# Optimization experiments

Measured on AMD Instinct MI355X. Metric: run time of the kernel, lower is better.

The kernel has to match this reference:

```python
import jax, jax.numpy as jnp
import numpy as np

B, S, D, H = 2, 2048, 1024, 16
DK = D // H

def setup_inputs() -> dict:
    key = jax.random.key(0)
    ks = jax.random.split(key, 11)
    scale = 1.0 / np.sqrt(D)
    inp = {
        'query': jax.random.normal(ks[0], (B, S, D), jnp.float32),
        'key':   jax.random.normal(ks[1], (B, S, D), jnp.float32),
        'value': jax.random.normal(ks[2], (B, S, D), jnp.float32),
        'wq': jax.random.normal(ks[3], (D, D), jnp.float32) * scale,
        'bq': jax.random.normal(ks[4], (D,), jnp.float32) * 0.01,
        'wk': jax.random.normal(ks[5], (D, D), jnp.float32) * scale,
        'bk': jax.random.normal(ks[6], (D,), jnp.float32) * 0.01,
        'wv': jax.random.normal(ks[7], (D, D), jnp.float32) * scale,
        'bv': jax.random.normal(ks[8], (D,), jnp.float32) * 0.01,
        'wo': jax.random.normal(ks[9], (D, D), jnp.float32) * scale,
        'bo': jax.random.normal(ks[10], (D,), jnp.float32) * 0.01,
    }
    return inp

def reference(query, key, value, wq, bq, wk, bk, wv, bv, wo, bo):
    nb = query.shape[0]
    # projections: torch nn.Linear computes x @ W^T + b; here weights stored as (in,out)
    def proj(x, w, b):
        return (x @ w + b).reshape(nb, -1, H, DK).transpose(0, 2, 1, 3)  # [B,H,S,dk]
    q = proj(query, wq, bq)
    k = proj(key, wk, bk)
    v = proj(value, wv, bv)
    scores = jnp.einsum('bhqd,bhkd->bhqk', q, k) / jnp.sqrt(jnp.float32(DK))
    p = jax.nn.softmax(scores, axis=-1)  # dropout p=0 (eval)
    x = jnp.einsum('bhqk,bhkd->bhqd', p, v)
    x = x.transpose(0, 2, 1, 3).reshape(nb, -1, H * DK)
    return x @ wo + bo
```

## Files before the change

kernel.cpp:

```cpp
#include <hip/hip_runtime.h>


typedef __attribute__((ext_vector_type(8))) __bf16 bf16x8;
typedef __attribute__((ext_vector_type(4))) __bf16 bf16x4;
typedef __attribute__((ext_vector_type(8))) float f32x8;
typedef __attribute__((ext_vector_type(4))) float f32x4;
typedef __attribute__((ext_vector_type(16))) float f32x16;
typedef unsigned uv2 __attribute__((ext_vector_type(2)));

#define MFMA16 __builtin_amdgcn_mfma_f32_16x16x32_bf16
#define MFMA32 __builtin_amdgcn_mfma_f32_32x32x16_bf16

union Bf8 { bf16x8 v; __bf16 e[8]; };

__device__ inline f32x4 zero4() { f32x4 z; z[0]=z[1]=z[2]=z[3]=0.f; return z; }
__device__ inline f32x16 zero16() {
    f32x16 z;
#pragma unroll
    for (int i = 0; i < 16; i++) z[i] = 0.f;
    return z;
}

__device__ inline float fast_exp2(float x) {
#if __has_builtin(__builtin_amdgcn_exp2f)
    return __builtin_amdgcn_exp2f(x);
#else
    return __expf(x * 0.6931471805599453f);
#endif
}

#if __has_builtin(__builtin_amdgcn_permlane32_swap)
#define HAVE_PLSWAP 1
#endif

__device__ inline void plswap32(unsigned &a, unsigned &b) {
#ifdef HAVE_PLSWAP
    uv2 r = __builtin_amdgcn_permlane32_swap(a, b, false, false);
    a = r[0]; b = r[1];
#else
    unsigned sa = __shfl_xor((int)a, 32), sb = __shfl_xor((int)b, 32);
    bool hi = (threadIdx.x & 32) != 0;
    unsigned na = hi ? sb : a;
    unsigned nb = hi ? b : sa;
    a = na; b = nb;
#endif
}

__device__ inline float red32_max(float x) {
#ifdef HAVE_PLSWAP
    unsigned a = __float_as_uint(x), b = __float_as_uint(x);
    uv2 r = __builtin_amdgcn_permlane32_swap(a, b, false, false);
    return fmaxf(__uint_as_float(r[0]), __uint_as_float(r[1]));
#else
    return fmaxf(x, __shfl_xor(x, 32));
#endif
}
__device__ inline float red32_sum(float x) {
#ifdef HAVE_PLSWAP
    unsigned a = __float_as_uint(x), b = __float_as_uint(x);
    uv2 r = __builtin_amdgcn_permlane32_swap(a, b, false, false);
    return __uint_as_float(r[0]) + __uint_as_float(r[1]);
#else
    return x + __shfl_xor(x, 32);
#endif
}

__device__ inline unsigned pk2(float a, float b) {
    union { unsigned u; __bf16 e[2]; } r;
    r.e[0] = (__bf16)a; r.e[1] = (__bf16)b;
    return r.u;
}

__device__ inline void load_lds16(const void* g, void* l) {
    __builtin_amdgcn_global_load_lds(
        (const __attribute__((address_space(1))) unsigned int*)g,
        (__attribute__((address_space(3))) unsigned int*)l, 16, 0, 0);
}

__global__ __launch_bounds__(256) void prep_all(
        const float* __restrict__ w0, const float* __restrict__ w1,
        const float* __restrict__ w2, const float* __restrict__ w3,
        const float* __restrict__ x0, const float* __restrict__ x1,
        const float* __restrict__ x2,
        __bf16* __restrict__ wt, __bf16* __restrict__ d0,
        __bf16* __restrict__ d1, __bf16* __restrict__ d2) {
    const int z = blockIdx.z, t = threadIdx.x;
    if (z < 4) {
        const float* src = z == 0 ? w0 : z == 1 ? w1 : z == 2 ? w2 : w3;
        __bf16* dst = wt + (size_t)z * 1048576;
        __shared__ float tile[32][33];
        const int tc = t & 31, tr = t >> 5;
        const int r0 = blockIdx.y * 32, c0 = blockIdx.x * 32;
#pragma unroll
        for (int i = 0; i < 4; i++) {
            int r = tr + i * 8;
            tile[r][tc] = src[(size_t)(r0 + r) * 1024 + c0 + tc];
        }
        __syncthreads();
#pragma unroll
        for (int i = 0; i < 4; i++) {
            int r = tr + i * 8;
            dst[(size_t)(c0 + r) * 1024 + r0 + tc] = (__bf16)tile[tc][r];
        }
    } else {
        const float* src = z == 4 ? x0 : z == 5 ? x1 : x2;
        __bf16* dst = z == 4 ? d0 : z == 5 ? d1 : d2;
        int bid = blockIdx.y * 32 + blockIdx.x;
        size_t g = ((size_t)bid * 256 + t) * 16;
#pragma unroll
        for (int h = 0; h < 2; h++) {
            f32x8 a = *(const f32x8*)&src[g + h * 8];
            Bf8 tmp;
#pragma unroll
            for (int j = 0; j < 8; j++) tmp.e[j] = (__bf16)a[j];
            *(bf16x8*)&dst[g + h * 8] = tmp.v;
        }
    }
}

template <int MODE, typename OutT>
__device__ inline void gemm_fast_core(__bf16* __restrict__ smem,
                                      const __bf16* __restrict__ A,
                                      const __bf16* __restrict__ Bt,
                                      const float* __restrict__ bias,
                                      OutT* __restrict__ out, float scale) {
    __bf16* As = smem;
    __bf16* Bs = smem + 8192;
    const int t = threadIdx.x;
    const int wave = t >> 6, lane = t & 63, lm = lane & 15, quad = lane >> 4;
    const int m0 = blockIdx.y * 128, n0 = blockIdx.x * 128;
    const int wm = (wave >> 1) * 64, wn = (wave & 1) * 64;

    f32x4 acc[4][4];
#pragma unroll
    for (int i = 0; i < 4; i++)
#pragma unroll
        for (int j = 0; j < 4; j++) acc[i][j] = zero4();

    for (int k0 = 0; k0 < 1024; k0 += 64) {
#pragma unroll
        for (int i = 0; i < 4; i++) {
            int s = i * 256 + t;
            int row = s >> 3, cb = (s & 7) ^ (row & 7);
            size_t goff = (size_t)row * 1024 + k0 + cb * 8;
            load_lds16(&A[(size_t)m0 * 1024 + goff],
                       &As[(size_t)(i * 256 + wave * 64) * 8]);
            load_lds16(&Bt[(size_t)n0 * 1024 + goff],
                       &Bs[(size_t)(i * 256 + wave * 64) * 8]);
        }
        __syncthreads();
#pragma unroll
        for (int ks = 0; ks < 2; ks++) {
            bf16x8 af[4], bfr[4];
#pragma unroll
            for (int mt = 0; mt < 4; mt++)
                af[mt] = *(const bf16x8*)&As[(wm + mt * 16 + lm) * 64 +
                                             (((ks * 4 + quad) ^ (lm & 7)) * 8)];
#pragma unroll
            for (int nt = 0; nt < 4; nt++)
                bfr[nt] = *(const bf16x8*)&Bs[(wn + nt * 16 + lm) * 64 +
                                              (((ks * 4 + quad) ^ (lm & 7)) * 8)];
#pragma unroll
            for (int mt = 0; mt < 4; mt++)
#pragma unroll
                for (int nt = 0; nt < 4; nt++)
                    acc[mt][nt] = MFMA16(af[mt], bfr[nt], acc[mt][nt], 0, 0, 0);
        }
        __syncthreads();
    }

    float bv4[4];
#pragma unroll
    for (int nt = 0; nt < 4; nt++) bv4[nt] = bias[n0 + wn + nt * 16 + lm];

    if (MODE == 2) {
#pragma unroll
        for (int mt = 0; mt < 4; mt++)
#pragma unroll
            for (int r = 0; r < 4; r++) {
                int rr = wm + mt * 16 + quad * 4 + r;
#pragma unroll
                for (int nt = 0; nt < 4; nt++) {
                    int c = wn + nt * 16 + lm;
                    smem[c * 128 + (rr ^ (8 * (c & 15)))] =
                        (__bf16)((acc[mt][nt][r] + bv4[nt]) * scale);
                }
            }
        __syncthreads();
        const int b = m0 >> 11;
#pragma unroll
        for (int it = 0; it < 8; it++) {
            int g = it * 256 + t;
            int c = g >> 4, gr = g & 15;
            bf16x8 v = *(const bf16x8*)&smem[c * 128 + ((gr * 8) ^ (8 * (c & 15)))];
            int col = n0 + c, hh = col >> 6, dk = col & 63;
            int sglob = (m0 & 2047) + gr * 8;
            size_t idx = (size_t)(b * 16 + hh) * 131072 + (size_t)dk * 2048 + sglob;
            *(bf16x8*)&out[idx] = v;
        }
    } else {
#pragma unroll
        for (int mt = 0; mt < 4; mt++) {
#pragma unroll
            for (int r = 0; r < 4; r++) {
                int row = m0 + wm + mt * 16 + quad * 4 + r;
#pragma unroll
                for (int nt = 0; nt < 4; nt++) {
                    int col = n0 + wn + nt * 16 + lm;
                    float val = (acc[mt][nt][r] + bv4[nt]) * scale;
                    size_t idx;
                    if (MODE == 0) {
                        idx = (size_t)row * 1024 + col;
                    } else {
                        int b = row >> 11, s = row & 2047, hh = col >> 6, dk = col & 63;
                        idx = (size_t)(b * 16 + hh) * 131072 + (size_t)s * 64 + dk;
                    }
                    out[idx] = (OutT)val;
                }
            }
        }
    }
}

__global__ __launch_bounds__(256) void proj_fast3(
        const __bf16* __restrict__ xq, const __bf16* __restrict__ xk,
        const __bf16* __restrict__ xv, const __bf16* __restrict__ WT,
        const float* __restrict__ bq, const float* __restrict__ bk,
        const float* __restrict__ bv,
        __bf16* __restrict__ Q, __bf16* __restrict__ K, __bf16* __restrict__ Vt) {
    __shared__ __bf16 smem[16384];
    int z = blockIdx.z;
    if (z == 0)
        gemm_fast_core<1, __bf16>(smem, xq, WT, bq, Q, 0.18033688f);
    else if (z == 1)
        gemm_fast_core<1, __bf16>(smem, xk, WT + 1048576, bk, K, 1.f);
    else
        gemm_fast_core<2, __bf16>(smem, xv, WT + 2097152, bv, Vt, 1.f);
}

__global__ __launch_bounds__(256) void out_proj_fast64(
        const __bf16* __restrict__ A, const __bf16* __restrict__ Bt,
        const float* __restrict__ bias, float* __restrict__ out) {
    __shared__ __bf16 As[8192];
    __shared__ __bf16 Bs[4096];
    const int t = threadIdx.x;
    const int wave = t >> 6, lane = t & 63, lm = lane & 15, quad = lane >> 4;
    const int m0 = blockIdx.y * 128, n0 = blockIdx.x * 64;
    const int wm = (wave >> 1) * 64, wn = (wave & 1) * 32;

    f32x4 acc[4][2];
#pragma unroll
    for (int i = 0; i < 4; i++) { acc[i][0] = zero4(); acc[i][1] = zero4(); }

    for (int k0 = 0; k0 < 1024; k0 += 64) {
#pragma unroll
        for (int i = 0; i < 4; i++) {
            int s = i * 256 + t;
            int row = s >> 3, cb = (s & 7) ^ (row & 7);
            load_lds16(&A[(size_t)(m0 + row) * 1024 + k0 + cb * 8],
                       &As[(size_t)(i * 256 + wave * 64) * 8]);
            if (i < 2)
                load_lds16(&Bt[(size_t)(n0 + row) * 1024 + k0 + cb * 8],
                           &Bs[(size_t)(i * 256 + wave * 64) * 8]);
        }
        __syncthreads();
#pragma unroll
        for (int ks = 0; ks < 2; ks++) {
            bf16x8 af[4], bfr[2];
#pragma unroll
            for (int mt = 0; mt < 4; mt++)
                af[mt] = *(const bf16x8*)&As[(wm + mt * 16 + lm) * 64 +
                                             (((ks * 4 + quad) ^ (lm & 7)) * 8)];
#pragma unroll
            for (int nt = 0; nt < 2; nt++)
                bfr[nt] = *(const bf16x8*)&Bs[(wn + nt * 16 + lm) * 64 +
                                              (((ks * 4 + quad) ^ (lm & 7)) * 8)];
#pragma unroll
            for (int mt = 0; mt < 4; mt++)
#pragma unroll
                for (int nt = 0; nt < 2; nt++)
                    acc[mt][nt] = MFMA16(af[mt], bfr[nt], acc[mt][nt], 0, 0, 0);
        }
        __syncthreads();
    }

    float bv2[2];
#pragma unroll
    for (int nt = 0; nt < 2; nt++) bv2[nt] = bias[n0 + wn + nt * 16 + lm];

#pragma unroll
    for (int mt = 0; mt < 4; mt++)
#pragma unroll
        for (int r = 0; r < 4; r++) {
            int row = m0 + wm + mt * 16 + quad * 4 + r;
#pragma unroll
            for (int nt = 0; nt < 2; nt++) {
                int col = n0 + wn + nt * 16 + lm;
                out[(size_t)row * 1024 + col] = acc[mt][nt][r] + bv2[nt];
            }
        }
}

__global__ __launch_bounds__(256, 2) void attn_kernel(
        const __bf16* __restrict__ Q, const __bf16* __restrict__ K,
        const __bf16* __restrict__ Vt, __bf16* __restrict__ O) {
    __shared__ __bf16 smem[16384];
    const int t = threadIdx.x;
    const int wave = t >> 6, lane = t & 63;
    const int l31 = lane & 31, h = lane >> 5;
    const int q0 = blockIdx.x * 128;
    const int bh = blockIdx.y;
    const size_t base = (size_t)bh * 131072;

    bf16x8 bq[4];
    {
        int qrow = q0 + wave * 32 + l31;
#pragma unroll
        for (int kst = 0; kst < 4; kst++)
            bq[kst] = *(const bf16x8*)&Q[base + (size_t)qrow * 64 + kst * 16 + h * 8];
    }

    unsigned fo[2][4];
#pragma unroll
    for (int m = 0; m < 2; m++)
#pragma unroll
        for (int k = 0; k < 4; k++)
            fo[m][k] = (unsigned)((m * 32 + l31) * 64 +
                       (((k * 2 + h) ^ (l31 & 7) ^ ((l31 >> 3) & 3)) * 8));

    unsigned kdst[2], ksrc[2], vsrc[2];
#pragma unroll
    for (int i = 0; i < 2; i++) {
        int s = i * 256 + t;
        int row = s >> 3, cb = (s & 7) ^ (row & 7) ^ ((row >> 3) & 3);
        kdst[i] = (unsigned)((i * 256 + wave * 64) * 8);
        ksrc[i] = (unsigned)(row * 64 + cb * 8);
        vsrc[i] = (unsigned)(row * 2048 + cb * 8);
    }

    float m_run = -1e30f, l_run = 0.f;
    f32x16 o_acc[2];
    o_acc[0] = zero16();
    o_acc[1] = zero16();
    bf16x8 bp[4];

#pragma unroll
    for (int i = 0; i < 2; i++)
        load_lds16(&K[base + ksrc[i]], &smem[kdst[i]]);
    __syncthreads();

    auto body = [&](int it, int cur) {
        const int kv0 = it * 64;
        if (it < 31) {
#pragma unroll
            for (int i = 0; i < 2; i++)
                load_lds16(&K[base + (size_t)(kv0 + 64) * 64 + ksrc[i]],
                           &smem[(cur ^ 1) * 4096 + kdst[i]]);
        }
#pragma unroll
        for (int i = 0; i < 2; i++)
            load_lds16(&Vt[base + (size_t)kv0 + vsrc[i]],
                       &smem[8192 + cur * 4096 + kdst[i]]);

        f32x16 sc[2];
        sc[0] = zero16();
        sc[1] = zero16();
        __builtin_amdgcn_s_setprio(1);
#pragma unroll
        for (int mtk = 0; mtk < 2; mtk++)
#pragma unroll
            for (int kst = 0; kst < 4; kst++) {
                bf16x8 ak = *(const bf16x8*)&smem[cur * 4096 + fo[mtk][kst]];
                sc[mtk] = MFMA32(ak, bq[kst], sc[mtk], 0, 0, 0);
            }
        if (it > 0) {
#pragma unroll
            for (int kb = 0; kb < 4; kb++)
#pragma unroll
                for (int mtd = 0; mtd < 2; mtd++) {
                    bf16x8 av = *(const bf16x8*)&smem[8192 + (cur ^ 1) * 4096 +
                                                      fo[mtd][kb]];
                    o_acc[mtd] = MFMA32(av, bp[kb], o_acc[mtd], 0, 0, 0);
                }
        }
        __builtin_amdgcn_s_setprio(0);

        float mx = sc[0][0];
#pragma unroll
        for (int mtk = 0; mtk < 2; mtk++)
#pragma unroll
            for (int r = 0; r < 16; r++) mx = fmaxf(mx, sc[mtk][r]);
        mx = red32_max(mx);
        float mo = m_run;
        if (__all(mx <= mo + 8.f)) {
            float su = 0.f;
#pragma unroll
            for (int mtk = 0; mtk < 2; mtk++)
#pragma unroll
                for (int r = 0; r < 16; r++) {
                    float p = fast_exp2(sc[mtk][r] - mo);
                    sc[mtk][r] = p;
                    su += p;
                }
            l_run += su;
        } else {
            float mn = fmaxf(mo, mx);
            float alpha = fast_exp2(mo - mn);
            m_run = mn;
            float su = 0.f;
#pragma unroll
            for (int mtk = 0; mtk < 2; mtk++)
#pragma unroll
                for (int r = 0; r < 16; r++) {
                    float p = fast_exp2(sc[mtk][r] - mn);
                    sc[mtk][r] = p;
                    su += p;
                }
            l_run = l_run * alpha + su;
#pragma unroll
            for (int mtd = 0; mtd < 2; mtd++)
#pragma unroll
                for (int r = 0; r < 16; r++) o_acc[mtd][r] *= alpha;
        }

#pragma unroll
        for (int kb = 0; kb < 4; kb++) {
            const int mt = kb >> 1, g = (kb & 1) * 2;
            unsigned A0 = pk2(sc[mt][g * 4 + 0], sc[mt][g * 4 + 1]);
            unsigned A1 = pk2(sc[mt][g * 4 + 2], sc[mt][g * 4 + 3]);
            unsigned B0 = pk2(sc[mt][g * 4 + 4], sc[mt][g * 4 + 5]);
            unsigned B1 = pk2(sc[mt][g * 4 + 6], sc[mt][g * 4 + 7]);
            plswap32(A0, B0);
            plswap32(A1, B1);
            union { unsigned u[4]; bf16x8 v; } bb;
            bb.u[0] = A0; bb.u[1] = A1; bb.u[2] = B0; bb.u[3] = B1;
            bp[kb] = bb.v;
        }

        __syncthreads();
    };

    for (int it = 0; it < 32; it += 2) {
        body(it, 0);
        body(it + 1, 1);
    }

    {
        __builtin_amdgcn_s_setprio(1);
#pragma unroll
        for (int kb = 0; kb < 4; kb++)
#pragma unroll
            for (int mtd = 0; mtd < 2; mtd++) {
                bf16x8 av = *(const bf16x8*)&smem[8192 + 4096 + fo[mtd][kb]];
                o_acc[mtd] = MFMA32(av, bp[kb], o_acc[mtd], 0, 0, 0);
            }
        __builtin_amdgcn_s_setprio(0);
    }
    __syncthreads();

    {
        float inv = 1.f / red32_sum(l_run);
        __bf16* Osc = &smem[wave * 2176];
#pragma unroll
        for (int mtd = 0; mtd < 2; mtd++)
#pragma unroll
            for (int c = 0; c < 4; c++) {
                bf16x4 pk4;
#pragma unroll
                for (int r2 = 0; r2 < 4; r2++)
                    pk4[r2] = (__bf16)(o_acc[mtd][c * 4 + r2] * inv);
                *(bf16x4*)&Osc[l31 * 68 + mtd * 32 + c * 8 + h * 4] = pk4;
            }
        __asm__ volatile("" ::: "memory");
        const int b = bh >> 4, hh = bh & 15;
        int ql = lane >> 1, half = lane & 1;
        int srow = q0 + wave * 32 + ql;
#pragma unroll
        for (int j = 0; j < 4; j++) {
            bf16x8 v = *(const bf16x8*)&Osc[ql * 68 + half * 32 + j * 8];
            *(bf16x8*)&O[(size_t)(b * 2048 + srow) * 1024 + hh * 64 + half * 32 + j * 8] = v;
        }
    }
}

extern "C" void kernel_launch(void* const* d_in, const int* in_sizes, int n_in,
                              void* d_out, int out_size, void* d_ws, size_t ws_size,
                              hipStream_t stream) {
    if (ws_size < ((size_t)40 << 20)) return;

    const float* query = (const float*)d_in[0];
    const float* key_  = (const float*)d_in[1];
    const float* value = (const float*)d_in[2];
    const float* wq = (const float*)d_in[3];
    const float* bq = (const float*)d_in[4];
    const float* wk = (const float*)d_in[5];
    const float* bk = (const float*)d_in[6];
    const float* wv = (const float*)d_in[7];
    const float* bv = (const float*)d_in[8];
    const float* wo = (const float*)d_in[9];
    const float* bo = (const float*)d_in[10];
    float* out = (float*)d_out;

    char* ws = (char*)d_ws;
    __bf16* WT  = (__bf16*)(ws);
    __bf16* Qw  = (__bf16*)(ws + ((size_t)8  << 20));
    __bf16* Kw  = (__bf16*)(ws + ((size_t)16 << 20));
    __bf16* Vtw = (__bf16*)(ws + ((size_t)24 << 20));
    __bf16* Ow  = (__bf16*)(ws + ((size_t)32 << 20));

    __bf16* Xq = Ow;
    __bf16* Xk = (__bf16*)d_out;
    __bf16* Xv = (__bf16*)d_out + 4194304;

    prep_all<<<dim3(32, 32, 7), dim3(256), 0, stream>>>(
        wq, wk, wv, wo, query, key_, value, WT, Xq, Xk, Xv);
    proj_fast3<<<dim3(8, 32, 3), dim3(256), 0, stream>>>(
        Xq, Xk, Xv, WT, bq, bk, bv, Qw, Kw, Vtw);
    attn_kernel<<<dim3(16, 32), dim3(256), 0, stream>>>(Qw, Kw, Vtw, Ow);
    out_proj_fast64<<<dim3(16, 32), dim3(256), 0, stream>>>(
        Ow, WT + 3 * 1048576, bo, out);
}
```

Baseline: 228.1 us.

## Split KV sequence across two wave teams per block and merge softmax partials

Doubles the attention block to 512 threads, with two 4-wave teams each processing half of the key/value sequence in separate LDS regions, then merges partial outputs using the log-sum-exp rescale through shared memory. The aim is to shorten the per-block serial KV loop and raise wave-level parallelism per CU. It also restructures the row max and sum reductions into tree form to shorten dependency chains. Costs are doubled LDS use, an extra merge pass with fp32 staging, and possibly fewer resident blocks.

```diff
diff --git a/kernel.cpp b/kernel.cpp
--- a/kernel.cpp
+++ b/kernel.cpp
@@ -301,20 +301,24 @@
         }
 }
 
-__global__ __launch_bounds__(256, 2) void attn_kernel(
+__global__ __launch_bounds__(512, 4) void attn_kernel(
         const __bf16* __restrict__ Q, const __bf16* __restrict__ K,
         const __bf16* __restrict__ Vt, __bf16* __restrict__ O) {
-    __shared__ __bf16 smem[16384];
+    __shared__ __bf16 smem[32768];
     const int t = threadIdx.x;
     const int wave = t >> 6, lane = t & 63;
     const int l31 = lane & 31, h = lane >> 5;
+    const int team = wave >> 2, w4 = wave & 3;
+    const int tt = t & 255;
+    const unsigned Tb = team * 16384;
+    const int kvbase = team * 1024;
     const int q0 = blockIdx.x * 128;
     const int bh = blockIdx.y;
     const size_t base = (size_t)bh * 131072;
 
     bf16x8 bq[4];
     {
-        int qrow = q0 + wave * 32 + l31;
+        int qrow = q0 + w4 * 32 + l31;
 #pragma unroll
         for (int kst = 0; kst < 4; kst++)
             bq[kst] = *(const bf16x8*)&Q[base + (size_t)qrow * 64 + kst * 16 + h * 8];
@@ -331,9 +335,9 @@
     unsigned kdst[2], ksrc[2], vsrc[2];
 #pragma unroll
     for (int i = 0; i < 2; i++) {
-        int s = i * 256 + t;
+        int s = i * 256 + tt;
         int row = s >> 3, cb = (s & 7) ^ (row & 7) ^ ((row >> 3) & 3);
-        kdst[i] = (unsigned)((i * 256 + wave * 64) * 8);
+        kdst[i] = Tb + (unsigned)((i * 256 + w4 * 64) * 8);
         ksrc[i] = (unsigned)(row * 64 + cb * 8);
         vsrc[i] = (unsigned)(row * 2048 + cb * 8);
     }
@@ -346,12 +350,12 @@
 
 #pragma unroll
     for (int i = 0; i < 2; i++)
-        load_lds16(&K[base + ksrc[i]], &smem[kdst[i]]);
+        load_lds16(&K[base + (size_t)kvbase * 64 + ksrc[i]], &smem[kdst[i]]);
     __syncthreads();
 
     auto body = [&](int it, int cur) {
-        const int kv0 = it * 64;
-        if (it < 31) {
+        const int kv0 = kvbase + it * 64;
+        if (it < 15) {
 #pragma unroll
             for (int i = 0; i < 2; i++)
                 load_lds16(&K[base + (size_t)(kv0 + 64) * 64 + ksrc[i]],
@@ -370,7 +374,7 @@
         for (int mtk = 0; mtk < 2; mtk++)
 #pragma unroll
             for (int kst = 0; kst < 4; kst++) {
-                bf16x8 ak = *(const bf16x8*)&smem[cur * 4096 + fo[mtk][kst]];
+                bf16x8 ak = *(const bf16x8*)&smem[Tb + cur * 4096 + fo[mtk][kst]];
                 sc[mtk] = MFMA32(ak, bq[kst], sc[mtk], 0, 0, 0);
             }
         if (it > 0) {
@@ -378,49 +382,52 @@
             for (int kb = 0; kb < 4; kb++)
 #pragma unroll
                 for (int mtd = 0; mtd < 2; mtd++) {
-                    bf16x8 av = *(const bf16x8*)&smem[8192 + (cur ^ 1) * 4096 +
+                    bf16x8 av = *(const bf16x8*)&smem[Tb + 8192 + (cur ^ 1) * 4096 +
                                                       fo[mtd][kb]];
                     o_acc[mtd] = MFMA32(av, bp[kb], o_acc[mtd], 0, 0, 0);
                 }
         }
         __builtin_amdgcn_s_setprio(0);
 
-        float mx = sc[0][0];
-#pragma unroll
-        for (int mtk = 0; mtk < 2; mtk++)
-#pragma unroll
-            for (int r = 0; r < 16; r++) mx = fmaxf(mx, sc[mtk][r]);
-        mx = red32_max(mx);
+        float tm16[16];
+#pragma unroll
+        for (int i = 0; i < 16; i++) tm16[i] = fmaxf(sc[0][i], sc[1][i]);
+#pragma unroll
+        for (int st = 8; st >= 1; st >>= 1)
+#pragma unroll
+            for (int i = 0; i < st; i++) tm16[i] = fmaxf(tm16[i], tm16[i + st]);
+        float mx = red32_max(tm16[0]);
         float mo = m_run;
         if (__all(mx <= mo + 8.f)) {
-            float su = 0.f;
 #pragma unroll
             for (int mtk = 0; mtk < 2; mtk++)
 #pragma unroll
-                for (int r = 0; r < 16; r++) {
-                    float p = fast_exp2(sc[mtk][r] - mo);
-                    sc[mtk][r] = p;
-                    su += p;
-                }
-            l_run += su;
+                for (int r = 0; r < 16; r++)
+                    sc[mtk][r] = fast_exp2(sc[mtk][r] - mo);
         } else {
             float mn = fmaxf(mo, mx);
             float alpha = fast_exp2(mo - mn);
             m_run = mn;
-            float su = 0.f;
 #pragma unroll
             for (int mtk = 0; mtk < 2; mtk++)
 #pragma unroll
-                for (int r = 0; r < 16; r++) {
-                    float p = fast_exp2(sc[mtk][r] - mn);
-                    sc[mtk][r] = p;
-                    su += p;
-                }
-            l_run = l_run * alpha + su;
+                for (int r = 0; r < 16; r++)
+                    sc[mtk][r] = fast_exp2(sc[mtk][r] - mn);
+            l_run *= alpha;
 #pragma unroll
             for (int mtd = 0; mtd < 2; mtd++)
 #pragma unroll
                 for (int r = 0; r < 16; r++) o_acc[mtd][r] *= alpha;
+        }
+        {
+            float s16[16];
+#pragma unroll
+            for (int i = 0; i < 16; i++) s16[i] = sc[0][i] + sc[1][i];
+#pragma unroll
+            for (int st = 8; st >= 1; st >>= 1)
+#pragma unroll
+                for (int i = 0; i < st; i++) s16[i] += s16[i + st];
+            l_run += s16[0];
         }
 
 #pragma unroll
@@ -440,7 +447,7 @@
         __syncthreads();
     };
 
-    for (int it = 0; it < 32; it += 2) {
+    for (int it = 0; it < 16; it += 2) {
         body(it, 0);
         body(it + 1, 1);
     }
@@ -451,30 +458,58 @@
         for (int kb = 0; kb < 4; kb++)
 #pragma unroll
             for (int mtd = 0; mtd < 2; mtd++) {
-                bf16x8 av = *(const bf16x8*)&smem[8192 + 4096 + fo[mtd][kb]];
+                bf16x8 av = *(const bf16x8*)&smem[Tb + 8192 + 4096 + fo[mtd][kb]];
                 o_acc[mtd] = MFMA32(av, bp[kb], o_acc[mtd], 0, 0, 0);
             }
         __builtin_amdgcn_s_setprio(0);
     }
     __syncthreads();
 
-    {
-        float inv = 1.f / red32_sum(l_run);
-        __bf16* Osc = &smem[wave * 2176];
+    float l_loc = red32_sum(l_run);
+    float m_loc = m_run;
+    float* fsm = (float*)smem;
+    const int qi = w4 * 32 + l31;
+    if (team == 1) {
+#pragma unroll
+        for (int mtd = 0; mtd < 2; mtd++)
+#pragma unroll
+            for (int c = 0; c < 4; c++)
+#pragma unroll
+                for (int r2 = 0; r2 < 4; r2++)
+                    fsm[qi * 68 + mtd * 32 + c * 8 + h * 4 + r2] =
+                        o_acc[mtd][c * 4 + r2];
+        if (h == 0) {
+            fsm[8704 + qi * 2]     = m_loc;
+            fsm[8704 + qi * 2 + 1] = l_loc;
+        }
+    }
+    __syncthreads();
+    if (team == 0) {
+        float m1 = fsm[8704 + qi * 2];
+        float l1 = fsm[8704 + qi * 2 + 1];
+        float mm = fmaxf(m_loc, m1);
+        float a0 = fast_exp2(m_loc - mm);
+        float a1 = fast_exp2(m1 - mm);
+        float linv = 1.f / (l_loc * a0 + l1 * a1);
+        a0 *= linv; a1 *= linv;
+        __bf16* Osc = &smem[17920 + w4 * 2176];
 #pragma unroll
         for (int mtd = 0; mtd < 2; mtd++)
 #pragma unroll
             for (int c = 0; c < 4; c++) {
                 bf16x4 pk4;
 #pragma unroll
-                for (int r2 = 0; r2 < 4; r2++)
-                    pk4[r2] = (__bf16)(o_acc[mtd][c * 4 + r2] * inv);
+                for (int r2 = 0; r2 < 4; r2++) {
+                    int d = mtd * 32 + c * 8 + h * 4 + r2;
+                    pk4[r2] = (__bf16)(o_acc[mtd][c * 4 + r2] * a0 +
+                                       fsm[qi * 68 + d] * a1);
+                }
                 *(bf16x4*)&Osc[l31 * 68 + mtd * 32 + c * 8 + h * 4] = pk4;
             }
         __asm__ volatile("" ::: "memory");
         const int b = bh >> 4, hh = bh & 15;
         int ql = lane >> 1, half = lane & 1;
-        int srow = q0 + wave * 32 + ql;
+        int srow = q0 + w4 * 32 + ql;
 #pragma unroll
         for (int j = 0; j < 4; j++) {
             bf16x8 v = *(const bf16x8*)&Osc[ql * 68 + half * 32 + j * 8];
@@ -516,7 +551,7 @@
         wq, wk, wv, wo, query, key_, value, WT, Xq, Xk, Xv);
     proj_fast3<<<dim3(8, 32, 3), dim3(256), 0, stream>>>(
         Xq, Xk, Xv, WT, bq, bk, bv, Qw, Kw, Vtw);
-    attn_kernel<<<dim3(16, 32), dim3(256), 0, stream>>>(Qw, Kw, Vtw, Ow);
+    attn_kernel<<<dim3(16, 32), dim3(512), 0, stream>>>(Qw, Kw, Vtw, Ow);
     out_proj_fast64<<<dim3(16, 32), dim3(256), 0, stream>>>(
         Ow, WT + 3 * 1048576, bo, out);
 }
```

New measurement: 328.3 us. +44.0%, slower.

## Replace per-tile max reduction with exp-first softmax and sum-triggered rescale

Applied to the files above, without the earlier changes.

Drops the per-tile row-max computation and cross-lane max reduction. Exponentials are computed directly against the running offset, and a rescale by the observed peak runs only when the tile sum exceeds a threshold. Also folds the per-tile LDS offsets into one array plus a constant, reducing register use. This removes a serial max-reduce from the softmax critical path. The trade-off is numerical risk: with no max subtraction, exp2 can overflow to inf before the threshold check fires, and if that happens, dividing by pmax gives NaN.

```diff
diff --git a/kernel.cpp b/kernel.cpp
--- a/kernel.cpp
+++ b/kernel.cpp
@@ -46,15 +46,6 @@
 #endif
 }
 
-__device__ inline float red32_max(float x) {
-#ifdef HAVE_PLSWAP
-    unsigned a = __float_as_uint(x), b = __float_as_uint(x);
-    uv2 r = __builtin_amdgcn_permlane32_swap(a, b, false, false);
-    return fmaxf(__uint_as_float(r[0]), __uint_as_float(r[1]));
-#else
-    return fmaxf(x, __shfl_xor(x, 32));
-#endif
-}
 __device__ inline float red32_sum(float x) {
 #ifdef HAVE_PLSWAP
     unsigned a = __float_as_uint(x), b = __float_as_uint(x);
@@ -320,13 +311,11 @@
             bq[kst] = *(const bf16x8*)&Q[base + (size_t)qrow * 64 + kst * 16 + h * 8];
     }
 
-    unsigned fo[2][4];
-#pragma unroll
-    for (int m = 0; m < 2; m++)
-#pragma unroll
-        for (int k = 0; k < 4; k++)
-            fo[m][k] = (unsigned)((m * 32 + l31) * 64 +
-                       (((k * 2 + h) ^ (l31 & 7) ^ ((l31 >> 3) & 3)) * 8));
+    unsigned fo[4];
+#pragma unroll
+    for (int k = 0; k < 4; k++)
+        fo[k] = (unsigned)(l31 * 64 +
+                (((k * 2 + h) ^ (l31 & 7) ^ ((l31 >> 3) & 3)) * 8));
 
     unsigned kdst[2], ksrc[2], vsrc[2];
 #pragma unroll
@@ -338,7 +327,7 @@
         vsrc[i] = (unsigned)(row * 2048 + cb * 8);
     }
 
-    float m_run = -1e30f, l_run = 0.f;
+    float m_run = 0.f, l_run = 0.f;
     f32x16 o_acc[2];
     o_acc[0] = zero16();
     o_acc[1] = zero16();
@@ -370,7 +359,7 @@
         for (int mtk = 0; mtk < 2; mtk++)
 #pragma unroll
             for (int kst = 0; kst < 4; kst++) {
-                bf16x8 ak = *(const bf16x8*)&smem[cur * 4096 + fo[mtk][kst]];
+                bf16x8 ak = *(const bf16x8*)&smem[cur * 4096 + mtk * 2048 + fo[kst]];
                 sc[mtk] = MFMA32(ak, bq[kst], sc[mtk], 0, 0, 0);
             }
         if (it > 0) {
@@ -379,49 +368,60 @@
 #pragma unroll
                 for (int mtd = 0; mtd < 2; mtd++) {
                     bf16x8 av = *(const bf16x8*)&smem[8192 + (cur ^ 1) * 4096 +
-                                                      fo[mtd][kb]];
+                                                      mtd * 2048 + fo[kb]];
                     o_acc[mtd] = MFMA32(av, bp[kb], o_acc[mtd], 0, 0, 0);
                 }
         }
         __builtin_amdgcn_s_setprio(0);
 
-        float mx = sc[0][0];
 #pragma unroll
         for (int mtk = 0; mtk < 2; mtk++)
 #pragma unroll
-            for (int r = 0; r < 16; r++) mx = fmaxf(mx, sc[mtk][r]);
-        mx = red32_max(mx);
-        float mo = m_run;
-        if (__all(mx <= mo + 8.f)) {
-            float su = 0.f;
+            for (int r = 0; r < 16; r++)
+                sc[mtk][r] = fast_exp2(sc[mtk][r] - m_run);
+        float tr8[8];
+#pragma unroll
+        for (int i = 0; i < 8; i++)
+            tr8[i] = (sc[0][i] + sc[0][i + 8]) + (sc[1][i] + sc[1][i + 8]);
+#pragma unroll
+        for (int st = 4; st >= 1; st >>= 1)
+#pragma unroll
+            for (int i = 0; i < st; i++) tr8[i] += tr8[i + st];
+        float su = tr8[0];
+        if (!__all(su <= 1048576.f)) {
+            float pm8[8];
+#pragma unroll
+            for (int i = 0; i < 8; i++)
+                pm8[i] = fmaxf(fmaxf(sc[0][i], sc[0][i + 8]),
+                               fmaxf(sc[1][i], sc[1][i + 8]));
+#pragma unroll
+            for (int st = 4; st >= 1; st >>= 1)
+#pragma unroll
+                for (int i = 0; i < st; i++) pm8[i] = fmaxf(pm8[i], pm8[i + st]);
+            float pmax = pm8[0];
+#ifdef HAVE_PLSWAP
+            {
+                unsigned a = __float_as_uint(pmax), b = a;
+                uv2 rr = __builtin_amdgcn_permlane32_swap(a, b, false, false);
+                pmax = fmaxf(__uint_as_float(rr[0]), __uint_as_float(rr[1]));
+            }
+#else
+            pmax = fmaxf(pmax, __shfl_xor(pmax, 32));
+#endif
+            float alpha = 1.f / pmax;
+            m_run += __log2f(pmax);
 #pragma unroll
             for (int mtk = 0; mtk < 2; mtk++)
 #pragma unroll
-                for (int r = 0; r < 16; r++) {
-                    float p = fast_exp2(sc[mtk][r] - mo);
-                    sc[mtk][r] = p;
-                    su += p;
-                }
-            l_run += su;
-        } else {
-            float mn = fmaxf(mo, mx);
-            float alpha = fast_exp2(mo - mn);
-            m_run = mn;
-            float su = 0.f;
-#pragma unroll
-            for (int mtk = 0; mtk < 2; mtk++)
-#pragma unroll
-                for (int r = 0; r < 16; r++) {
-                    float p = fast_exp2(sc[mtk][r] - mn);
-                    sc[mtk][r] = p;
-                    su += p;
-                }
-            l_run = l_run * alpha + su;
+                for (int r = 0; r < 16; r++) sc[mtk][r] *= alpha;
 #pragma unroll
             for (int mtd = 0; mtd < 2; mtd++)
 #pragma unroll
                 for (int r = 0; r < 16; r++) o_acc[mtd][r] *= alpha;
-        }
+            l_run *= alpha;
+            su *= alpha;
+        }
+        l_run += su;
 
 #pragma unroll
         for (int kb = 0; kb < 4; kb++) {
@@ -451,7 +451,7 @@
         for (int kb = 0; kb < 4; kb++)
 #pragma unroll
             for (int mtd = 0; mtd < 2; mtd++) {
-                bf16x8 av = *(const bf16x8*)&smem[8192 + 4096 + fo[mtd][kb]];
+                bf16x8 av = *(const bf16x8*)&smem[8192 + 4096 + mtd * 2048 + fo[kb]];
                 o_acc[mtd] = MFMA32(av, bp[kb], o_acc[mtd], 0, 0, 0);
             }
         __builtin_amdgcn_s_setprio(0);
```

Result: no change. 224.2 us (-1.7%).
